# Performance work log

Measured on AMD Instinct MI355X. Metric: run time of the kernel, lower is better.

Reference implementation:

```python
import jax, jax.numpy as jnp
import numpy as np

N_EMBD = 768
N_HEAD = 12
HEAD_DIM = N_EMBD // N_HEAD
EPS = 1e-5


def _ln(x, g, b):
    mu = jnp.mean(x, axis=-1, keepdims=True)
    var = jnp.mean(jnp.square(x - mu), axis=-1, keepdims=True)
    return (x - mu) * jax.lax.rsqrt(var + EPS) * g + b


def _gelu(x):
    # GPT-2 / BERT tanh-approximate GELU (new_gelu)
    c = jnp.sqrt(2.0 / jnp.pi).astype(x.dtype)
    return 0.5 * x * (1.0 + jnp.tanh(c * (x + 0.044715 * x * x * x)))


def setup_inputs() -> dict:
    key = jax.random.key(0)
    ks = jax.random.split(key, 8)
    B, T, C = 4, 2048, N_EMBD
    s = 0.02
    return {
        "x": jax.random.normal(ks[0], (B, T, C), jnp.float32),
        "attention_mask": jnp.ones((B, T), jnp.float32),
        "ln1_g": jnp.ones((C,), jnp.float32),
        "ln1_b": jnp.zeros((C,), jnp.float32),
        "ln2_g": jnp.ones((C,), jnp.float32),
        "ln2_b": jnp.zeros((C,), jnp.float32),
        "W_attn": jax.random.normal(ks[1], (C, 3 * C), jnp.float32) * s,
        "b_attn": jnp.zeros((3 * C,), jnp.float32),
        "W_proj": jax.random.normal(ks[2], (C, C), jnp.float32) * s,
        "b_proj": jnp.zeros((C,), jnp.float32),
        "W_fc": jax.random.normal(ks[3], (C, 4 * C), jnp.float32) * s,
        "b_fc": jnp.zeros((4 * C,), jnp.float32),
        "W_out": jax.random.normal(ks[4], (4 * C, C), jnp.float32) * s,
        "b_out": jnp.zeros((C,), jnp.float32),
    }


def reference(x, attention_mask, ln1_g, ln1_b, ln2_g, ln2_b,
              W_attn, b_attn, W_proj, b_proj, W_fc, b_fc, W_out, b_out):
    B, T, C = x.shape
    H, D = N_HEAD, HEAD_DIM

    # --- attention sublayer ---
    h = _ln(x, ln1_g, ln1_b)
    qkv = h @ W_attn + b_attn                      # [B,T,3C]
    q, k, v = jnp.split(qkv, 3, axis=-1)
    q = q.reshape(B, T, H, D).transpose(0, 2, 1, 3)  # [B,H,T,D]
    k = k.reshape(B, T, H, D).transpose(0, 2, 1, 3)
    v = v.reshape(B, T, H, D).transpose(0, 2, 1, 3)

    att = jnp.einsum('bhqd,bhkd->bhqk', q, k) * (1.0 / jnp.sqrt(D).astype(x.dtype))
    mask_add = (1.0 - attention_mask)[:, None, None, :] * -10000.0  # [B,1,1,T]
    att = att + mask_add
    att = jax.nn.softmax(att, axis=-1)
    y = jnp.einsum('bhqk,bhkd->bhqd', att, v)      # [B,H,T,D]
    y = y.transpose(0, 2, 1, 3).reshape(B, T, C)
    x = x + (y @ W_proj + b_proj)

    # --- MLP sublayer ---
    h = _ln(x, ln2_g, ln2_b)
    h = _gelu(h @ W_fc + b_fc)
    x = x + (h @ W_out + b_out)
    return x
```

## Files before the change

kernel.cpp:

```cpp
#include <hip/hip_runtime.h>
#include <hip/hip_bf16.h>
#include <cstdint>

using short8   = __attribute__((ext_vector_type(8))) short;
using floatx4  = __attribute__((ext_vector_type(4))) float;
using float2v  = __attribute__((ext_vector_type(2))) float;
using ushort4v = __attribute__((ext_vector_type(4))) unsigned short;

#define DEVI static __device__ __forceinline__

DEVI unsigned short f2bf(float f) {
    union { float f; unsigned u; } v; v.f = f;
    unsigned r = v.u + 0x7FFFu + ((v.u >> 16) & 1u);
    return (unsigned short)(r >> 16);
}

DEVI unsigned cvtpk_bf16(float lo, float hi) {
    unsigned r;
    asm("v_cvt_pk_bf16_f32 %0, %1, %2" : "=v"(r) : "v"(lo), "v"(hi));
    return r;
}

typedef const __attribute__((address_space(1))) unsigned int gas_uint;
typedef __attribute__((address_space(3))) unsigned int las_uint;

DEVI void gload16(const void* g, void* l) {
    __builtin_amdgcn_global_load_lds((gas_uint*)g, (las_uint*)l, 16, 0, 0);
}

DEVI float gelu_f(float x) {
    float z = 0.7978845608028654f * (x + 0.044715f * x * x * x);
    float e = __expf(2.0f * z);
    float t = 1.0f - 2.0f / (e + 1.0f);
    return 0.5f * x * (1.0f + t);
}

#define QSCALE 0.18033688011112042f

__global__ __launch_bounds__(256)
void transpose_cast(const float* __restrict__ W, unsigned short* __restrict__ Wt,
                    int K, int N)
{
    __shared__ float tile[32][33];
    const int n0 = blockIdx.x * 32, k0 = blockIdx.y * 32;
    const int tx = threadIdx.x & 31, ty = threadIdx.x >> 5;
#pragma unroll
    for (int j = 0; j < 4; ++j)
        tile[ty + j * 8][tx] = W[(long)(k0 + ty + j * 8) * N + n0 + tx];
    __syncthreads();
#pragma unroll
    for (int j = 0; j < 4; ++j)
        Wt[(long)(n0 + ty + j * 8) * K + k0 + tx] = f2bf(tile[tx][ty + j * 8]);
}

__global__ __launch_bounds__(256)
void ln_cast_k(const float* __restrict__ x, const float* __restrict__ g,
               const float* __restrict__ beta, unsigned short* __restrict__ out)
{
    const int row = blockIdx.x;
    const int tid = threadIdx.x;
    const float* xr = x + (long)row * 768;
    float v0 = xr[tid], v1 = xr[tid + 256], v2 = xr[tid + 512];
    float s  = v0 + v1 + v2;
    float sq = v0 * v0 + v1 * v1 + v2 * v2;
#pragma unroll
    for (int m = 1; m < 64; m <<= 1) {
        s  += __shfl_xor(s, m);
        sq += __shfl_xor(sq, m);
    }
    __shared__ float ss[4], ssq[4];
    if ((tid & 63) == 0) { ss[tid >> 6] = s; ssq[tid >> 6] = sq; }
    __syncthreads();
    s  = ss[0] + ss[1] + ss[2] + ss[3];
    sq = ssq[0] + ssq[1] + ssq[2] + ssq[3];
    const float mean = s * (1.0f / 768.0f);
    const float var  = sq * (1.0f / 768.0f) - mean * mean;
    const float rstd = rsqrtf(var + 1e-5f);
    unsigned short* orow = out + (long)row * 768;
    orow[tid]       = f2bf((v0 - mean) * rstd * g[tid]       + beta[tid]);
    orow[tid + 256] = f2bf((v1 - mean) * rstd * g[tid + 256] + beta[tid + 256]);
    orow[tid + 512] = f2bf((v2 - mean) * rstd * g[tid + 512] + beta[tid + 512]);
}

template<int EPI>
__global__ __launch_bounds__(256)
void gemm128(const unsigned short* __restrict__ A,
             const unsigned short* __restrict__ Bt,
             const float* __restrict__ bias,
             const float* __restrict__ resid,
             unsigned short* __restrict__ ob0,
             unsigned short* __restrict__ ob1,
             unsigned short* __restrict__ ob2,
             float* __restrict__ of,
             int K, int N)
{
    const int mt = blockIdx.x, nt = blockIdx.y;
    const int tid = threadIdx.x;
    const int w = tid >> 6, lane = tid & 63;
    const int l16 = lane & 15, lq = lane >> 4;
    const int wm = w >> 1, wn = w & 1;

    __shared__ unsigned short As[128 * 64];
    __shared__ unsigned short Bs[128 * 64];

    const floatx4 fzero = {0.f, 0.f, 0.f, 0.f};
    floatx4 acc[4][4];
#pragma unroll
    for (int i = 0; i < 4; ++i)
#pragma unroll
        for (int j = 0; j < 4; ++j) acc[i][j] = fzero;

    const char* Abyte = (const char*)A + (long)mt * 128 * K * 2;
    const char* Bbyte = (const char*)Bt + (long)nt * 128 * K * 2;
    const int KT = K >> 6;

    for (int kt = 0; kt < KT; ++kt) {
        const int kbyte = kt * 128;
#pragma unroll
        for (int r4 = 0; r4 < 4; ++r4) {
            int base = (w * 4 + r4) * 1024;
            int loff = base + lane * 16;
            int row  = loff >> 7;
            int scb  = (loff & 127) ^ ((row & 7) << 4);
            gload16(Abyte + (long)row * (K * 2) + kbyte + scb, (char*)As + base);
            gload16(Bbyte + (long)row * (K * 2) + kbyte + scb, (char*)Bs + base);
        }
        __syncthreads();
#pragma unroll
        for (int ks = 0; ks < 2; ++ks) {
            const int kb = ks * 64 + lq * 16;
            short8 af[4], bfr[4];
#pragma unroll
            for (int f = 0; f < 4; ++f) {
                int ar = wm * 64 + f * 16 + l16;
                af[f]  = *(const short8*)((const char*)As + ar * 128 + (kb ^ ((ar & 7) << 4)));
                int br = wn * 64 + f * 16 + l16;
                bfr[f] = *(const short8*)((const char*)Bs + br * 128 + (kb ^ ((br & 7) << 4)));
            }
#pragma unroll
            for (int i = 0; i < 4; ++i)
#pragma unroll
                for (int j = 0; j < 4; ++j)
                    acc[i][j] = __builtin_amdgcn_mfma_f32_16x16x32_bf16(af[i], bfr[j], acc[i][j], 0, 0, 0);
        }
        __syncthreads();
    }

    const int col0 = nt * 128 + wn * 64;
    const int row0 = mt * 128 + wm * 64;
#pragma unroll
    for (int j = 0; j < 4; ++j) {
        const int col = col0 + j * 16 + l16;
        const float bv = bias[col];
#pragma unroll
        for (int i = 0; i < 4; ++i) {
            const int rowb = row0 + i * 16 + lq * 4;
            float v[4];
#pragma unroll
            for (int r = 0; r < 4; ++r) v[r] = acc[i][j][r] + bv;

            if (EPI == 0) {
                const int which = (col >= 1536) ? 2 : (col >= 768 ? 1 : 0);
                const int c = col - which * 768;
                const int hh = c >> 6, d = c & 63;
                const int bb = rowb >> 11;
                const int t  = rowb & 2047;
                if (which == 2) {
                    ushort4v pk;
#pragma unroll
                    for (int r = 0; r < 4; ++r) pk[r] = f2bf(v[r]);
                    const int tlo = t & 31;
                    const int tS  = (t & ~31) + ((tlo & 12) << 1) + ((tlo & 16) >> 2);
                    long vi = ((long)(bb * 12 + hh) * 64 + d) * 2048 + tS;
                    *(ushort4v*)(ob2 + vi) = pk;
                } else {
                    unsigned short* dst = (which == 0) ? ob0 : ob1;
                    const float qs = (which == 0) ? QSCALE : 1.0f;
                    long base = ((long)(bb * 12 + hh) * 2048 + t) * 64 + d;
#pragma unroll
                    for (int r = 0; r < 4; ++r) dst[base + (long)r * 64] = f2bf(v[r] * qs);
                }
            } else if (EPI == 1 || EPI == 3) {
#pragma unroll
                for (int r = 0; r < 4; ++r) {
                    long idx = (long)(rowb + r) * N + col;
                    of[idx] = v[r] + resid[idx];
                }
            } else {
#pragma unroll
                for (int r = 0; r < 4; ++r) {
                    long idx = (long)(rowb + r) * N + col;
                    ob0[idx] = f2bf(gelu_f(v[r]));
                }
            }
        }
    }
}

__global__ __launch_bounds__(512)
void attn_fwd(const unsigned short* __restrict__ q,
              const unsigned short* __restrict__ k,
              const unsigned short* __restrict__ vt,
              const float* __restrict__ mask,
              unsigned short* __restrict__ y)
{
    const int qt = blockIdx.x;
    const int bh = blockIdx.y;
    const int b = bh / 12, h = bh - b * 12;
    const int tid = threadIdx.x;
    const int w = tid >> 6, lane = tid & 63;
    const int l16 = lane & 15, lq = lane >> 4;

    __shared__ unsigned short Ks[128 * 64];
    __shared__ unsigned short Vs[64 * 128];
    __shared__ float madd[128];
    __shared__ int mq;

    if (tid == 0) mq = 0;
    __syncthreads();
    {
        const float* mrow = mask + (long)b * 2048 + tid * 4;
        int bad = 0;
#pragma unroll
        for (int j = 0; j < 4; ++j) bad |= (mrow[j] != 1.0f);
        if (bad) atomicOr(&mq, 1);
    }

    const unsigned short* qrow = q + ((long)bh * 2048 + qt * 128 + w * 16 + l16) * 64;
    const short8 qf0 = *(const short8*)(qrow + lq * 8);
    const short8 qf1 = *(const short8*)(qrow + 32 + lq * 8);

    const char* kg = (const char*)(k + (long)bh * 2048 * 64);
    const char* vg = (const char*)(vt + (long)bh * 64 * 2048);
    int koff[2], voff[2], lb[2];
#pragma unroll
    for (int r2 = 0; r2 < 2; ++r2) {
        int loff = r2 * 8192 + tid * 16;
        int rowK = loff >> 7;
        koff[r2] = rowK * 128 + ((loff & 127) ^ ((rowK & 7) << 4));
        int rowV = loff >> 8;
        voff[r2] = rowV * 4096 + ((loff & 255) ^ ((rowV & 7) << 4));
        lb[r2]   = loff;
    }

    __syncthreads();
    const bool usemask = (mq != 0);

    const floatx4 fzero = {0.f, 0.f, 0.f, 0.f};
    floatx4 accO[4];
#pragma unroll
    for (int n = 0; n < 4; ++n) accO[n] = fzero;
    float m2 = -1e30f, lsum = 0.f;

    for (int kt = 0; kt < 16; ++kt) {
        const char* kgt = kg + (long)kt * 16384;
        const char* vgt = vg + kt * 256;
#pragma unroll
        for (int r2 = 0; r2 < 2; ++r2) {
            gload16(kgt + koff[r2], (char*)Ks + lb[r2]);
            gload16(vgt + voff[r2], (char*)Vs + lb[r2]);
        }
        if (usemask && tid < 128)
            madd[tid] = (1.0f - mask[b * 2048 + kt * 128 + tid]) * (-10000.0f * 1.4426950408889634f);
        __syncthreads();

        floatx4 st[8];
#pragma unroll
        for (int f = 0; f < 8; ++f) st[f] = fzero;
        __builtin_amdgcn_s_setprio(1);
#pragma unroll
        for (int f = 0; f < 8; ++f) {
            const int kr = f * 16 + l16;
            const int sw = (kr & 7) << 4;
            short8 ka0 = *(const short8*)((const char*)Ks + kr * 128 + ((lq * 16) ^ sw));
            short8 ka1 = *(const short8*)((const char*)Ks + kr * 128 + ((64 + lq * 16) ^ sw));
            st[f] = __builtin_amdgcn_mfma_f32_16x16x32_bf16(ka0, qf0, st[f], 0, 0, 0);
            st[f] = __builtin_amdgcn_mfma_f32_16x16x32_bf16(ka1, qf1, st[f], 0, 0, 0);
        }
        __builtin_amdgcn_s_setprio(0);

        if (usemask) {
#pragma unroll
            for (int f = 0; f < 8; ++f) {
                floatx4 md = *(const floatx4*)((const char*)madd + f * 64 + lq * 16);
                st[f] += md;
            }
        }

        float2v lo[8], hi[8];
#pragma unroll
        for (int f = 0; f < 8; ++f) {
            lo[f][0] = st[f][0]; lo[f][1] = st[f][1];
            hi[f][0] = st[f][2]; hi[f][1] = st[f][3];
        }

        float2v mx = __builtin_elementwise_max(lo[0], hi[0]);
#pragma unroll
        for (int f = 1; f < 8; ++f)
            mx = __builtin_elementwise_max(mx, __builtin_elementwise_max(lo[f], hi[f]));
        float rm = fmaxf(mx[0], mx[1]);
        rm = fmaxf(rm, __shfl_xor(rm, 16));
        rm = fmaxf(rm, __shfl_xor(rm, 32));

        if (!__all(rm <= m2 + 8.0f)) {
            const float mn = fmaxf(m2, rm);
            const float corr = exp2f(m2 - mn);
            m2 = mn;
            lsum *= corr;
            floatx4 cv;
            cv[0] = __shfl(corr, lq * 4 + 0);
            cv[1] = __shfl(corr, lq * 4 + 1);
            cv[2] = __shfl(corr, lq * 4 + 2);
            cv[3] = __shfl(corr, lq * 4 + 3);
#pragma unroll
            for (int n = 0; n < 4; ++n) accO[n] *= cv;
        }

        const float2v m2v = {m2, m2};
        float2v rs2 = {0.f, 0.f};
        unsigned pw[16];
#pragma unroll
        for (int f = 0; f < 8; ++f) {
            float2v d0 = lo[f] - m2v;
            float2v d1 = hi[f] - m2v;
            float2v e0, e1;
            e0[0] = exp2f(d0[0]); e0[1] = exp2f(d0[1]);
            e1[0] = exp2f(d1[0]); e1[1] = exp2f(d1[1]);
            rs2 += e0;
            rs2 += e1;
            pw[f * 2]     = cvtpk_bf16(e0[0], e0[1]);
            pw[f * 2 + 1] = cvtpk_bf16(e1[0], e1[1]);
        }
        float rs = rs2[0] + rs2[1];
        rs += __shfl_xor(rs, 16);
        rs += __shfl_xor(rs, 32);
        lsum += rs;

        __builtin_amdgcn_s_setprio(1);
#pragma unroll
        for (int c = 0; c < 4; ++c) {
            union { unsigned u[4]; short8 s8; } pu;
            pu.u[0] = pw[c * 4 + 0];
            pu.u[1] = pw[c * 4 + 1];
            pu.u[2] = pw[c * 4 + 2];
            pu.u[3] = pw[c * 4 + 3];
            const int kb2 = c * 64 + lq * 16;
#pragma unroll
            for (int n = 0; n < 4; ++n) {
                const int vr = n * 16 + l16;
                short8 vb = *(const short8*)((const char*)Vs + vr * 256 + (kb2 ^ ((vr & 7) << 4)));
                accO[n] = __builtin_amdgcn_mfma_f32_16x16x32_bf16(pu.s8, vb, accO[n], 0, 0, 0);
            }
        }
        __builtin_amdgcn_s_setprio(0);
        __syncthreads();
    }

    const float li = 1.0f / lsum;
    floatx4 lv;
    lv[0] = __shfl(li, lq * 4 + 0);
    lv[1] = __shfl(li, lq * 4 + 1);
    lv[2] = __shfl(li, lq * 4 + 2);
    lv[3] = __shfl(li, lq * 4 + 3);
    unsigned short* ybase = y + ((long)(b * 2048 + qt * 128 + w * 16 + lq * 4)) * 768 + h * 64;
#pragma unroll
    for (int r = 0; r < 4; ++r) {
        unsigned short* yrow = ybase + (long)r * 768;
#pragma unroll
        for (int n = 0; n < 4; ++n)
            yrow[n * 16 + l16] = f2bf(accO[n][r] * lv[r]);
    }
}

extern "C" void kernel_launch(void* const* d_in, const int* in_sizes, int n_in,
                              void* d_out, int out_size, void* d_ws, size_t ws_size,
                              hipStream_t stream)
{
    const float* x     = (const float*)d_in[0];
    const float* amask = (const float*)d_in[1];
    const float* ln1g  = (const float*)d_in[2];
    const float* ln1b  = (const float*)d_in[3];
    const float* ln2g  = (const float*)d_in[4];
    const float* ln2b  = (const float*)d_in[5];
    const float* Wattn = (const float*)d_in[6];
    const float* battn = (const float*)d_in[7];
    const float* Wproj = (const float*)d_in[8];
    const float* bproj = (const float*)d_in[9];
    const float* Wfc   = (const float*)d_in[10];
    const float* bfc   = (const float*)d_in[11];
    const float* Wout  = (const float*)d_in[12];
    const float* bout  = (const float*)d_in[13];
    float* out = (float*)d_out;

    char* ws = (char*)d_ws;
    unsigned short* wt_attn = (unsigned short*)ws;  ws += (long)2304 * 768 * 2;
    unsigned short* wt_proj = (unsigned short*)ws;  ws += (long)768 * 768 * 2;
    unsigned short* wt_fc   = (unsigned short*)ws;  ws += (long)3072 * 768 * 2;
    unsigned short* wt_out  = (unsigned short*)ws;  ws += (long)768 * 3072 * 2;
    unsigned short* hbuf    = (unsigned short*)ws;  ws += (long)8192 * 768 * 2;
    unsigned short* qbuf    = (unsigned short*)ws;  ws += (long)48 * 2048 * 64 * 2;
    unsigned short* kbuf    = (unsigned short*)ws;  ws += (long)48 * 2048 * 64 * 2;
    unsigned short* vtbuf   = (unsigned short*)ws;  ws += (long)48 * 2048 * 64 * 2;
    unsigned short* ybuf    = (unsigned short*)ws;  ws += (long)8192 * 768 * 2;
    unsigned short* hfc     = (unsigned short*)ws;  ws += (long)8192 * 3072 * 2;

    transpose_cast<<<dim3(2304 / 32, 768 / 32), 256, 0, stream>>>(Wattn, wt_attn, 768, 2304);
    transpose_cast<<<dim3(768 / 32, 768 / 32), 256, 0, stream>>>(Wproj, wt_proj, 768, 768);
    transpose_cast<<<dim3(3072 / 32, 768 / 32), 256, 0, stream>>>(Wfc, wt_fc, 768, 3072);
    transpose_cast<<<dim3(768 / 32, 3072 / 32), 256, 0, stream>>>(Wout, wt_out, 3072, 768);

    ln_cast_k<<<8192, 256, 0, stream>>>(x, ln1g, ln1b, hbuf);

    gemm128<0><<<dim3(64, 18), 256, 0, stream>>>(hbuf, wt_attn, battn, nullptr,
                                                 qbuf, kbuf, vtbuf, nullptr, 768, 2304);

    attn_fwd<<<dim3(16, 48), 512, 0, stream>>>(qbuf, kbuf, vtbuf, amask, ybuf);

    gemm128<1><<<dim3(64, 6), 256, 0, stream>>>(ybuf, wt_proj, bproj, x,
                                                nullptr, nullptr, nullptr, out, 768, 768);

    ln_cast_k<<<8192, 256, 0, stream>>>(out, ln2g, ln2b, hbuf);

    gemm128<2><<<dim3(64, 24), 256, 0, stream>>>(hbuf, wt_fc, bfc, nullptr,
                                                 hfc, nullptr, nullptr, nullptr, 768, 3072);

    gemm128<3><<<dim3(64, 6), 256, 0, stream>>>(hfc, wt_out, bout, out,
                                                nullptr, nullptr, nullptr, out, 3072, 768);
}
```

Measured before the change: 329.7 us.

## Use 128x64 tiles for N=768 GEMMs and add XCD-aware block swizzle

Adds a gemm_n64 kernel with 128x64 output tiles for the projection and MLP-out GEMMs, where N=768. This doubles the workgroup count from 384 to 768 so the GPU's compute units are better filled. It also remaps workgroup IDs across the 8 XCDs so neighbouring tiles share an L2, applied both to the new kernel and to gemm128. The cost is smaller tiles with less data reuse per workgroup and more redundant A-tile loads.

Result: faster. 318.4 us (-3.4%).

```diff
diff --git a/kernel.cpp b/kernel.cpp
--- a/kernel.cpp
+++ b/kernel.cpp
@@ -33,6 +33,13 @@
     float e = __expf(2.0f * z);
     float t = 1.0f - 2.0f / (e + 1.0f);
     return 0.5f * x * (1.0f + t);
+}
+
+DEVI int xcd_swizzle(int gX) {
+    const int nwg = gX * gridDim.y;
+    const int orig = blockIdx.y * gX + blockIdx.x;
+    if (nwg & 7) return orig;
+    return (orig & 7) * (nwg >> 3) + (orig >> 3);
 }
 
 #define QSCALE 0.18033688011112042f
@@ -87,14 +94,14 @@
 void gemm128(const unsigned short* __restrict__ A,
              const unsigned short* __restrict__ Bt,
              const float* __restrict__ bias,
-             const float* __restrict__ resid,
              unsigned short* __restrict__ ob0,
              unsigned short* __restrict__ ob1,
              unsigned short* __restrict__ ob2,
-             float* __restrict__ of,
              int K, int N)
 {
-    const int mt = blockIdx.x, nt = blockIdx.y;
+    const int wg = xcd_swizzle(gridDim.x);
+    const int gY = gridDim.y;
+    const int mt = wg / gY, nt = wg % gY;
     const int tid = threadIdx.x;
     const int w = tid >> 6, lane = tid & 63;
     const int l16 = lane & 15, lq = lane >> 4;
@@ -180,18 +187,103 @@
 #pragma unroll
                     for (int r = 0; r < 4; ++r) dst[base + (long)r * 64] = f2bf(v[r] * qs);
                 }
-            } else if (EPI == 1 || EPI == 3) {
-#pragma unroll
-                for (int r = 0; r < 4; ++r) {
-                    long idx = (long)(rowb + r) * N + col;
-                    of[idx] = v[r] + resid[idx];
-                }
             } else {
 #pragma unroll
                 for (int r = 0; r < 4; ++r) {
                     long idx = (long)(rowb + r) * N + col;
                     ob0[idx] = f2bf(gelu_f(v[r]));
                 }
+            }
+        }
+    }
+}
+
+__global__ __launch_bounds__(256)
+void gemm_n64(const unsigned short* __restrict__ A,
+              const unsigned short* __restrict__ Bt,
+              const float* __restrict__ bias,
+              const float* __restrict__ resid,
+              float* __restrict__ of,
+              int K, int N)
+{
+    const int wg = xcd_swizzle(gridDim.x);
+    const int gY = gridDim.y;
+    const int mt = wg / gY, nt = wg % gY;
+    const int tid = threadIdx.x;
+    const int w = tid >> 6, lane = tid & 63;
+    const int l16 = lane & 15, lq = lane >> 4;
+    const int wm = w >> 1, wn = w & 1;
+
+    __shared__ unsigned short As[128 * 64];
+    __shared__ unsigned short Bs[64 * 64];
+
+    const floatx4 fzero = {0.f, 0.f, 0.f, 0.f};
+    floatx4 acc[4][2];
+#pragma unroll
+    for (int i = 0; i < 4; ++i)
+#pragma unroll
+        for (int j = 0; j < 2; ++j) acc[i][j] = fzero;
+
+    const int K2 = K * 2;
+    const char* Abyte = (const char*)A + (long)mt * 128 * K2;
+    const char* Bbyte = (const char*)Bt + (long)nt * 64 * K2;
+    const int KT = K >> 6;
+
+    for (int kt = 0; kt < KT; ++kt) {
+        const int kbyte = kt * 128;
+#pragma unroll
+        for (int r4 = 0; r4 < 4; ++r4) {
+            int base = (w * 4 + r4) * 1024;
+            int loff = base + lane * 16;
+            int row  = loff >> 7;
+            int scb  = (loff & 127) ^ ((row & 7) << 4);
+            gload16(Abyte + (long)row * K2 + kbyte + scb, (char*)As + base);
+        }
+#pragma unroll
+        for (int r2 = 0; r2 < 2; ++r2) {
+            int base = (w * 2 + r2) * 1024;
+            int loff = base + lane * 16;
+            int row  = loff >> 7;
+            int scb  = (loff & 127) ^ ((row & 7) << 4);
+            gload16(Bbyte + (long)row * K2 + kbyte + scb, (char*)Bs + base);
+        }
+        __syncthreads();
+#pragma unroll
+        for (int ks = 0; ks < 2; ++ks) {
+            const int kb = ks * 64 + lq * 16;
+            short8 af[4], bfr[2];
+#pragma unroll
+            for (int f = 0; f < 4; ++f) {
+                int ar = wm * 64 + f * 16 + l16;
+                af[f] = *(const short8*)((const char*)As + ar * 128 + (kb ^ ((ar & 7) << 4)));
+            }
+#pragma unroll
+            for (int f = 0; f < 2; ++f) {
+                int br = wn * 32 + f * 16 + l16;
+                bfr[f] = *(const short8*)((const char*)Bs + br * 128 + (kb ^ ((br & 7) << 4)));
+            }
+#pragma unroll
+            for (int i = 0; i < 4; ++i)
+#pragma unroll
+                for (int j = 0; j < 2; ++j)
+                    acc[i][j] = __builtin_amdgcn_mfma_f32_16x16x32_bf16(af[i], bfr[j], acc[i][j], 0, 0, 0);
+        }
+        __syncthreads();
+    }
+
+    const int col0 = nt * 64 + wn * 32;
+    const int row0 = mt * 128 + wm * 64;
+#pragma unroll
+    for (int j = 0; j < 2; ++j) {
+        const int col = col0 + j * 16 + l16;
+        const float bv = bias[col];
+#pragma unroll
+        for (int i = 0; i < 4; ++i) {
+            const int rowb = row0 + i * 16 + lq * 4;
+#pragma unroll
+            for (int r = 0; r < 4; ++r) {
+                long idx = (long)(rowb + r) * N + col;
+                of[idx] = acc[i][j][r] + bv + resid[idx];
             }
         }
     }
@@ -411,19 +503,17 @@
 
     ln_cast_k<<<8192, 256, 0, stream>>>(x, ln1g, ln1b, hbuf);
 
-    gemm128<0><<<dim3(64, 18), 256, 0, stream>>>(hbuf, wt_attn, battn, nullptr,
-                                                 qbuf, kbuf, vtbuf, nullptr, 768, 2304);
+    gemm128<0><<<dim3(64, 18), 256, 0, stream>>>(hbuf, wt_attn, battn,
+                                                 qbuf, kbuf, vtbuf, 768, 2304);
 
     attn_fwd<<<dim3(16, 48), 512, 0, stream>>>(qbuf, kbuf, vtbuf, amask, ybuf);
 
-    gemm128<1><<<dim3(64, 6), 256, 0, stream>>>(ybuf, wt_proj, bproj, x,
-                                                nullptr, nullptr, nullptr, out, 768, 768);
+    gemm_n64<<<dim3(64, 12), 256, 0, stream>>>(ybuf, wt_proj, bproj, x, out, 768, 768);
 
     ln_cast_k<<<8192, 256, 0, stream>>>(out, ln2g, ln2b, hbuf);
 
-    gemm128<2><<<dim3(64, 24), 256, 0, stream>>>(hbuf, wt_fc, bfc, nullptr,
-                                                 hfc, nullptr, nullptr, nullptr, 768, 3072);
-
-    gemm128<3><<<dim3(64, 6), 256, 0, stream>>>(hfc, wt_out, bout, out,
-                                                nullptr, nullptr, nullptr, out, 3072, 768);
-}
+    gemm128<2><<<dim3(64, 24), 256, 0, stream>>>(hbuf, wt_fc, bfc,
+                                                 hfc, nullptr, nullptr, 768, 3072);
+
+    gemm_n64<<<dim3(64, 12), 256, 0, stream>>>(hfc, wt_out, bout, out, out, 3072, 768);
+}
```
